# Kernel optimization log

Hardware: AMD Instinct MI355X
Metric: run time of the kernel (lower is better)

The kernel has to match this reference:

```python
import jax, jax.numpy as jnp
import numpy as np


def conv2d(x, w, b, pad=0, groups=1):
    y = jax.lax.conv_general_dilated(
        x, w, (1, 1), [(pad, pad), (pad, pad)],
        dimension_numbers=('NCHW', 'OIHW', 'NCHW'), feature_group_count=groups)
    return y + b[None, :, None, None]


def layernorm(x, w, b, eps=1e-5):
    # per-pixel LayerNorm over channel dim (matches to_3d -> nn.LayerNorm(dim) -> to_4d)
    mu = x.mean(1, keepdims=True)
    var = ((x - mu) ** 2).mean(1, keepdims=True)
    return (x - mu) * jax.lax.rsqrt(var + eps) * w[None, :, None, None] + b[None, :, None, None]


def setup_inputs():
    key = jax.random.key(0)
    ks = jax.random.split(key, 16)
    B, C, H, W = 1, 64, 64, 64
    heads, dh = 8, 8
    inner = heads * dh          # 64
    hid_lc = 32                 # max(16, inner // 2)
    hid_f = 4 * C               # 256, ffn_expansion_factor = 4
    def s(k, shape, fan):
        return (jax.random.normal(k, shape, jnp.float32) / np.float32(np.sqrt(fan)))
    return {
        'x': jax.random.normal(ks[0], (B, C, H, W), jnp.float32),
        'luma': jax.random.uniform(ks[1], (B, 1, H, W), jnp.float32),
        'ln1_w': jnp.ones((C,), jnp.float32), 'ln1_b': jnp.zeros((C,), jnp.float32),
        'qkv_w': s(ks[2], (3 * inner, C, 1, 1), C), 'qkv_b': jnp.zeros((3 * inner,), jnp.float32),
        'proj_w': s(ks[3], (C, inner, 1, 1), inner), 'proj_b': jnp.zeros((C,), jnp.float32),
        'lc1_w': s(ks[4], (hid_lc, 1, 3, 3), 9), 'lc1_b': jnp.zeros((hid_lc,), jnp.float32),
        'lc2_w': s(ks[5], (hid_lc, hid_lc, 3, 3), 9 * hid_lc), 'lc2_b': jnp.zeros((hid_lc,), jnp.float32),
        'gam_w': s(ks[6], (inner, hid_lc, 1, 1), hid_lc), 'gam_b': jnp.zeros((inner,), jnp.float32),
        'bet_w': s(ks[7], (inner, hid_lc, 1, 1), hid_lc), 'bet_b': jnp.zeros((inner,), jnp.float32),
        'alpha': jnp.float32(0.1),
        'ln2_w': jnp.ones((C,), jnp.float32), 'ln2_b': jnp.zeros((C,), jnp.float32),
        'ffn1_w': s(ks[8], (hid_f, C, 1, 1), C), 'ffn1_b': jnp.zeros((hid_f,), jnp.float32),
        'dw_w': s(ks[9], (hid_f, 1, 3, 3), 9), 'dw_b': jnp.zeros((hid_f,), jnp.float32),
        'ffn2_w': s(ks[10], (C, hid_f, 1, 1), hid_f), 'ffn2_b': jnp.zeros((C,), jnp.float32),
    }


def reference(x, luma, ln1_w, ln1_b, qkv_w, qkv_b, proj_w, proj_b,
              lc1_w, lc1_b, lc2_w, lc2_b, gam_w, gam_b, bet_w, bet_b, alpha,
              ln2_w, ln2_b, ffn1_w, ffn1_b, dw_w, dw_b, ffn2_w, ffn2_b):
    B, C, H, W = x.shape
    heads = 8
    N = H * W
    # --- attention branch ---
    xn = layernorm(x, ln1_w, ln1_b)
    qkv = conv2d(xn, qkv_w, qkv_b)             # [B, 3*inner, H, W]
    inner = qkv.shape[1] // 3
    dh = inner // heads

    def to_bhnd(t):  # b (h d) x y -> b h (x y) d
        return t.reshape(B, heads, dh, N).transpose(0, 1, 3, 2)

    q, k, v = [to_bhnd(t) for t in jnp.split(qkv, 3, axis=1)]
    # luma conditioning
    h1 = jax.nn.relu(conv2d(luma, lc1_w, lc1_b, pad=1))
    h1 = jax.nn.relu(conv2d(h1, lc2_w, lc2_b, pad=1))
    g = to_bhnd(conv2d(h1, gam_w, gam_b))
    bt = to_bhnd(conv2d(h1, bet_w, bet_b))
    q = g * q + bt
    k = g * k + bt
    v = g * v + bt
    # additive luma bias on q (avg_pool2d 3x3, count_include_pad=True -> fixed /9)
    invL = 1.0 - luma
    invL = jax.lax.reduce_window(invL, 0.0, jax.lax.add, (1, 1, 3, 3), (1, 1, 1, 1),
                                 [(0, 0), (0, 0), (1, 1), (1, 1)]) / 9.0
    invL = invL.reshape(B, N)
    invL = invL - invL.mean(-1, keepdims=True)
    q = q + alpha * invL[:, None, :, None]
    scale = dh ** -0.5
    attn = jax.nn.softmax(jnp.einsum('bhid,bhjd->bhij', q, k) * scale, axis=-1)
    out = jnp.einsum('bhij,bhjd->bhid', attn, v)
    out = out.transpose(0, 1, 3, 2).reshape(B, inner, H, W)
    x = x + conv2d(out, proj_w, proj_b)
    # --- ConvFFN branch ---
    y = layernorm(x, ln2_w, ln2_b)
    y = conv2d(y, ffn1_w, ffn1_b)
    y = conv2d(y, dw_w, dw_b, pad=1, groups=y.shape[1])
    y = jax.nn.gelu(y, approximate=False)
    y = conv2d(y, ffn2_w, ffn2_b)
    return x + y
```

## Files before the change

kernel.cpp:

```cpp
#include <hip/hip_runtime.h>
#include <math.h>

#define NPIX 4096
#define IMG 64

typedef __attribute__((ext_vector_type(8))) short bf16x8;
typedef __attribute__((ext_vector_type(4))) float floatx4;
typedef __attribute__((ext_vector_type(4))) unsigned int uintx4;

__device__ __forceinline__ unsigned int split_pack(float x) {
  unsigned int u = __float_as_uint(x);
  unsigned int hif = u & 0xffff0000u;
  float lof = x - __uint_as_float(hif);
  return (u >> 16) | (__float_as_uint(lof) & 0xffff0000u);
}

__device__ __forceinline__ unsigned int hi_pair(float a, float b) {
  return (__float_as_uint(a) >> 16) | (__float_as_uint(b) & 0xffff0000u);
}

__global__ __launch_bounds__(256) void lc1_kernel(
    const float* __restrict__ luma, const float* __restrict__ w1,
    const float* __restrict__ b1, float* __restrict__ h1,
    float* __restrict__ pooled, float* __restrict__ bsums,
    unsigned short* __restrict__ cbuf) {
  __shared__ float red[256];
  int tile = blockIdx.x, ocg = blockIdx.y;
  int tid = threadIdx.x;
  if (tile == 0 && ocg == 0 && tid < 16) cbuf[tid] = (tid < 8) ? 0x3F80 : 0;
  int p = tile * 256 + tid;
  int py = p >> 6, px = p & 63;
  float v[9];
#pragma unroll
  for (int dy = 0; dy < 3; dy++)
#pragma unroll
    for (int dx = 0; dx < 3; dx++) {
      int y = py + dy - 1, x = px + dx - 1;
      v[dy * 3 + dx] =
          (y >= 0 && y < IMG && x >= 0 && x < IMG) ? luma[y * IMG + x] : 0.f;
    }
#pragma unroll
  for (int o = 0; o < 4; o++) {
    int oc = ocg * 4 + o;
    float s = b1[oc];
#pragma unroll
    for (int t = 0; t < 9; t++) s = fmaf(w1[oc * 9 + t], v[t], s);
    h1[oc * NPIX + p] = fmaxf(s, 0.f);
  }
  if (ocg == 0) {
    float sv = 0.f;
#pragma unroll
    for (int t = 0; t < 9; t++) sv += v[t];
    float cy = 3.f - (py == 0 ? 1.f : 0.f) - (py == 63 ? 1.f : 0.f);
    float cx = 3.f - (px == 0 ? 1.f : 0.f) - (px == 63 ? 1.f : 0.f);
    float pv = (cy * cx - sv) * (1.f / 9.f);
    pooled[p] = pv;
    red[tid] = pv;
    __syncthreads();
    for (int st = 128; st > 0; st >>= 1) {
      if (tid < st) red[tid] += red[tid + st];
      __syncthreads();
    }
    if (tid == 0) bsums[tile] = red[0];
  }
}

__global__ __launch_bounds__(256) void lc2_kernel(
    const float* __restrict__ h1, const float* __restrict__ w2,
    const float* __restrict__ b2, const float* __restrict__ x,
    float* __restrict__ h2, float* __restrict__ mu1, float* __restrict__ rs1) {
  __shared__ float tin[32][324];
  __shared__ float swt[4][32][9];
  int tile = blockIdx.x, ocg = blockIdx.y;
  int ty0 = (tile >> 2) * 16, tx0 = (tile & 3) * 16;
  int tid = threadIdx.x;
  for (int idx = tid; idx < 32 * 324; idx += 256) {
    int ic = idx / 324, pos = idx - ic * 324;
    int py = pos / 18, px = pos - py * 18;
    int gy = ty0 + py - 1, gx = tx0 + px - 1;
    tin[ic][pos] = (gy >= 0 && gy < IMG && gx >= 0 && gx < IMG)
                       ? h1[ic * NPIX + gy * IMG + gx]
                       : 0.f;
  }
  for (int idx = tid; idx < 4 * 32 * 9; idx += 256) {
    int o = idx / 288, r = idx - o * 288;
    swt[o][r / 9][r % 9] = w2[(ocg * 4 + o) * 288 + r];
  }
  __syncthreads();
  int ly = tid >> 4, lx = tid & 15;
  int p = (ty0 + ly) * IMG + tx0 + lx;
  float acc[4];
#pragma unroll
  for (int o = 0; o < 4; o++) acc[o] = b2[ocg * 4 + o];
  for (int ic = 0; ic < 32; ic++) {
    float v[9];
#pragma unroll
    for (int dy = 0; dy < 3; dy++)
#pragma unroll
      for (int dx = 0; dx < 3; dx++)
        v[dy * 3 + dx] = tin[ic][(ly + dy) * 18 + lx + dx];
#pragma unroll
    for (int o = 0; o < 4; o++)
#pragma unroll
      for (int t = 0; t < 9; t++) acc[o] = fmaf(swt[o][ic][t], v[t], acc[o]);
  }
#pragma unroll
  for (int o = 0; o < 4; o++)
    h2[(ocg * 4 + o) * NPIX + p] = fmaxf(acc[o], 0.f);
  if (ocg == 0) {
    float s = 0.f, q = 0.f;
#pragma unroll 8
    for (int cc = 0; cc < 64; cc++) {
      float xv = x[cc * NPIX + p];
      s += xv;
      q = fmaf(xv, xv, q);
    }
    float mu = s * (1.f / 64.f);
    mu1[p] = mu;
    rs1[p] = rsqrtf(q * (1.f / 64.f) - mu * mu + 1e-5f);
  }
}

__global__ __launch_bounds__(256) void ln_qkv_kernel(
    const float* __restrict__ X, const float* __restrict__ mu1,
    const float* __restrict__ rs1, const float* __restrict__ lnw,
    const float* __restrict__ lnb, const float* __restrict__ W,
    const float* __restrict__ bias, const float* __restrict__ gamW,
    const float* __restrict__ gamB, const float* __restrict__ betW,
    const float* __restrict__ betB, const float* __restrict__ h2,
    const float* __restrict__ pooled, const float* __restrict__ bsums,
    const float* __restrict__ alpha, unsigned short* __restrict__ qhl,
    unsigned short* __restrict__ khl, unsigned short* __restrict__ vthx,
    unsigned short* __restrict__ vtlx) {
  const float QSCALE = 0.35355339059327376f * 1.4426950408889634f;
  __shared__ float xs[64][64];
  __shared__ float wsh[64][64];
  __shared__ float h2s[32][64];
  __shared__ float wgs[32][64];
  __shared__ float wbs[32][64];
  __shared__ float mu[64];
  __shared__ float rs[64];
  int n0 = blockIdx.x * 64, part = blockIdx.y, m0 = part * 64;
  int tid = threadIdx.x;
  int c = tid >> 2, pg = (tid & 3) * 16;
  if (tid < 64) {
    mu[tid] = mu1[n0 + tid];
    rs[tid] = rs1[n0 + tid];
  }
  {
    const float4* src = (const float4*)&X[c * NPIX + n0 + pg];
    float4* dst = (float4*)&xs[c][pg];
    dst[0] = src[0]; dst[1] = src[1]; dst[2] = src[2]; dst[3] = src[3];
  }
  {
    int m = tid >> 2, kg = (tid & 3) * 16;
    const float4* wr = (const float4*)&W[(m0 + m) * 64 + kg];
    float4 w0 = wr[0], w1 = wr[1], w2 = wr[2], w3 = wr[3];
    float wv[16] = {w0.x, w0.y, w0.z, w0.w, w1.x, w1.y, w1.z, w1.w,
                    w2.x, w2.y, w2.z, w2.w, w3.x, w3.y, w3.z, w3.w};
#pragma unroll
    for (int j = 0; j < 16; j++) wsh[kg + j][m] = wv[j];
  }
  {
    int i0 = tid * 2;
    int k = i0 >> 4, nf = (i0 & 15) * 4;
    *(float4*)&h2s[k][nf] = *(const float4*)&h2[k * NPIX + n0 + nf];
    int i1 = i0 + 1;
    int k1 = i1 >> 4, nf1 = (i1 & 15) * 4;
    *(float4*)&h2s[k1][nf1] = *(const float4*)&h2[k1 * NPIX + n0 + nf1];
  }
  {
    int m = tid >> 2, kg = (tid & 3) * 8;
    const float4* g0 = (const float4*)&gamW[m * 32 + kg];
    float4 a = g0[0], b4 = g0[1];
    float gv[8] = {a.x, a.y, a.z, a.w, b4.x, b4.y, b4.z, b4.w};
#pragma unroll
    for (int j = 0; j < 8; j++) wgs[kg + j][m] = gv[j];
    const float4* bb0 = (const float4*)&betW[m * 32 + kg];
    float4 c4 = bb0[0], d4 = bb0[1];
    float bv[8] = {c4.x, c4.y, c4.z, c4.w, d4.x, d4.y, d4.z, d4.w};
#pragma unroll
    for (int j = 0; j < 8; j++) wbs[kg + j][m] = bv[j];
  }
  __syncthreads();
  {
    float wc = lnw[c], bc = lnb[c];
#pragma unroll
    for (int j = 0; j < 16; j++) {
      int p = pg + j;
      xs[c][p] = (xs[c][p] - mu[p]) * rs[p] * wc + bc;
    }
  }
  __syncthreads();
  int tx = tid & 15, ty = tid >> 4;
  float ga[4][4] = {}, ba[4][4] = {};
#pragma unroll 8
  for (int kk = 0; kk < 32; kk++) {
    float4 wg4 = *(const float4*)&wgs[kk][ty * 4];
    float4 wb4 = *(const float4*)&wbs[kk][ty * 4];
    float4 h24 = *(const float4*)&h2s[kk][tx * 4];
    float gv[4] = {wg4.x, wg4.y, wg4.z, wg4.w};
    float bv[4] = {wb4.x, wb4.y, wb4.z, wb4.w};
    float hv[4] = {h24.x, h24.y, h24.z, h24.w};
#pragma unroll
    for (int im = 0; im < 4; im++)
#pragma unroll
      for (int in = 0; in < 4; in++) {
        ga[im][in] = fmaf(gv[im], hv[in], ga[im][in]);
        ba[im][in] = fmaf(bv[im], hv[in], ba[im][in]);
      }
  }
#pragma unroll
  for (int im = 0; im < 4; im++) {
    int cc = ty * 4 + im;
    float gb = gamB[cc], bb2 = betB[cc];
#pragma unroll
    for (int in = 0; in < 4; in++) {
      ga[im][in] += gb;
      ba[im][in] += bb2;
    }
  }
  float acc[4][4] = {};
#pragma unroll 8
  for (int kk = 0; kk < 64; kk++) {
    float4 a = *(const float4*)&wsh[kk][ty * 4];
    float4 b4 = *(const float4*)&xs[kk][tx * 4];
    float av[4] = {a.x, a.y, a.z, a.w};
    float bv[4] = {b4.x, b4.y, b4.z, b4.w};
#pragma unroll
    for (int im = 0; im < 4; im++)
#pragma unroll
      for (int in = 0; in < 4; in++)
        acc[im][in] = fmaf(av[im], bv[in], acc[im][in]);
  }
  float val[4][4];
#pragma unroll
  for (int im = 0; im < 4; im++) {
    int cc = ty * 4 + im;
    float bv = bias[m0 + cc];
#pragma unroll
    for (int in = 0; in < 4; in++)
      val[im][in] = fmaf(ga[im][in], acc[im][in] + bv, ba[im][in]);
  }
  if (part == 0) {
    float msum = 0.f;
#pragma unroll
    for (int t = 0; t < 16; t++) msum += bsums[t];
    float mean = msum * (1.f / 4096.f);
    float a0 = alpha[0];
    const float4 pv = *(const float4*)&pooled[n0 + tx * 4];
    float iv[4] = {a0 * (pv.x - mean), a0 * (pv.y - mean),
                   a0 * (pv.z - mean), a0 * (pv.w - mean)};
#pragma unroll
    for (int im = 0; im < 4; im++)
#pragma unroll
      for (int in = 0; in < 4; in++)
        val[im][in] = (val[im][in] + iv[in]) * QSCALE;
  }
  if (part < 2) {
    unsigned short* dst = (part == 0) ? qhl : khl;
    int h = ty >> 1, d0 = (ty & 1) * 4;
#pragma unroll
    for (int in = 0; in < 4; in++) {
      int n = n0 + tx * 4 + in;
      unsigned int pk[4];
#pragma unroll
      for (int im = 0; im < 4; im++) pk[im] = split_pack(val[im][in]);
      short4 hi, lo;
      hi.x = (short)(pk[0] & 0xffffu); hi.y = (short)(pk[1] & 0xffffu);
      hi.z = (short)(pk[2] & 0xffffu); hi.w = (short)(pk[3] & 0xffffu);
      lo.x = (short)(pk[0] >> 16); lo.y = (short)(pk[1] >> 16);
      lo.z = (short)(pk[2] >> 16); lo.w = (short)(pk[3] >> 16);
      unsigned short* base = dst + ((size_t)(h * NPIX + n) << 4) + d0;
      *(short4*)base = hi;
      *(short4*)(base + 8) = lo;
    }
  } else {
    int nq = n0 + tx * 4;
    int off0 = (nq >> 5) * 32 + ((nq >> 4) & 1) * 4 + ((nq >> 2) & 3) * 8;
#pragma unroll
    for (int im = 0; im < 4; im++) {
      int cc = ty * 4 + im;
      unsigned int pk[4];
#pragma unroll
      for (int in = 0; in < 4; in++) pk[in] = split_pack(val[im][in]);
      short4 hi, lo;
      hi.x = (short)(pk[0] & 0xffffu); hi.y = (short)(pk[1] & 0xffffu);
      hi.z = (short)(pk[2] & 0xffffu); hi.w = (short)(pk[3] & 0xffffu);
      lo.x = (short)(pk[0] >> 16); lo.y = (short)(pk[1] >> 16);
      lo.z = (short)(pk[2] >> 16); lo.w = (short)(pk[3] >> 16);
      *(short4*)(vthx + (size_t)cc * NPIX + off0) = hi;
      *(short4*)(vtlx + (size_t)cc * NPIX + off0) = lo;
    }
  }
}

__global__ __launch_bounds__(256, 4) void attn_kernel(
    const unsigned short* __restrict__ qhl,
    const unsigned short* __restrict__ khl,
    const unsigned short* __restrict__ vthx,
    const unsigned short* __restrict__ vtlx,
    const unsigned short* __restrict__ cbuf, float* __restrict__ pacc,
    float* __restrict__ pl) {
  int tid = threadIdx.x;
  int wave = tid >> 6, lane = tid & 63;
  int g = lane >> 4, c = lane & 15;
  int h = blockIdx.y, jp = blockIdx.z;
  int i0 = blockIdx.x * 128 + wave * 32;
  int jbase = jp * 1024;
  const bf16x8 qB0 = *(const bf16x8*)(qhl + ((size_t)(h * NPIX + i0 + c) << 4) +
                                      ((g & 1) << 3));
  const bf16x8 qB1 = *(const bf16x8*)(
      qhl + ((size_t)(h * NPIX + i0 + 16 + c) << 4) + ((g & 1) << 3));
  const unsigned short* kp =
      khl + ((size_t)(h * NPIX + jbase + c) << 4) + ((g >> 1) << 3);
  const unsigned short* vhp;
  const unsigned short* vlp;
  int vstep;
  if (c < 8) {
    vhp = vthx + (size_t)(h * 8 + c) * NPIX + jbase + (g << 3);
    vlp = vtlx + (size_t)(h * 8 + c) * NPIX + jbase + (g << 3);
    vstep = 32;
  } else {
    vhp = (c == 8) ? cbuf : (cbuf + 8);
    vlp = cbuf + 8;
    vstep = 0;
  }
  floatx4 zero4 = {0.f, 0.f, 0.f, 0.f};
  floatx4 aH0 = zero4, aM0 = zero4, aH1 = zero4, aM1 = zero4;
#pragma unroll 2
  for (int jt = 0; jt < 32; ++jt) {
    bf16x8 ka0 = *(const bf16x8*)kp;
    bf16x8 ka1 = *(const bf16x8*)(kp + 256);
    bf16x8 avh = *(const bf16x8*)vhp;
    bf16x8 avl = *(const bf16x8*)vlp;
    kp += 512;
    vhp += vstep;
    vlp += vstep;
    floatx4 s00 =
        __builtin_amdgcn_mfma_f32_16x16x32_bf16(ka0, qB0, zero4, 0, 0, 0);
    floatx4 s01 =
        __builtin_amdgcn_mfma_f32_16x16x32_bf16(ka1, qB0, zero4, 0, 0, 0);
    floatx4 s10 =
        __builtin_amdgcn_mfma_f32_16x16x32_bf16(ka0, qB1, zero4, 0, 0, 0);
    floatx4 s11 =
        __builtin_amdgcn_mfma_f32_16x16x32_bf16(ka1, qB1, zero4, 0, 0, 0);
    {
      float p0 = __builtin_amdgcn_exp2f(fminf(s00[0], 80.f));
      float p1 = __builtin_amdgcn_exp2f(fminf(s00[1], 80.f));
      float p2 = __builtin_amdgcn_exp2f(fminf(s00[2], 80.f));
      float p3 = __builtin_amdgcn_exp2f(fminf(s00[3], 80.f));
      float p4 = __builtin_amdgcn_exp2f(fminf(s01[0], 80.f));
      float p5 = __builtin_amdgcn_exp2f(fminf(s01[1], 80.f));
      float p6 = __builtin_amdgcn_exp2f(fminf(s01[2], 80.f));
      float p7 = __builtin_amdgcn_exp2f(fminf(s01[3], 80.f));
      uintx4 bh;
      bh.x = hi_pair(p0, p1);
      bh.y = hi_pair(p2, p3);
      bh.z = hi_pair(p4, p5);
      bh.w = hi_pair(p6, p7);
      bf16x8 pbh = __builtin_bit_cast(bf16x8, bh);
      aH0 = __builtin_amdgcn_mfma_f32_16x16x32_bf16(avh, pbh, aH0, 0, 0, 0);
      aM0 = __builtin_amdgcn_mfma_f32_16x16x32_bf16(avl, pbh, aM0, 0, 0, 0);
    }
    {
      float p0 = __builtin_amdgcn_exp2f(fminf(s10[0], 80.f));
      float p1 = __builtin_amdgcn_exp2f(fminf(s10[1], 80.f));
      float p2 = __builtin_amdgcn_exp2f(fminf(s10[2], 80.f));
      float p3 = __builtin_amdgcn_exp2f(fminf(s10[3], 80.f));
      float p4 = __builtin_amdgcn_exp2f(fminf(s11[0], 80.f));
      float p5 = __builtin_amdgcn_exp2f(fminf(s11[1], 80.f));
      float p6 = __builtin_amdgcn_exp2f(fminf(s11[2], 80.f));
      float p7 = __builtin_amdgcn_exp2f(fminf(s11[3], 80.f));
      uintx4 bh;
      bh.x = hi_pair(p0, p1);
      bh.y = hi_pair(p2, p3);
      bh.z = hi_pair(p4, p5);
      bh.w = hi_pair(p6, p7);
      bf16x8 pbh = __builtin_bit_cast(bf16x8, bh);
      aH1 = __builtin_amdgcn_mfma_f32_16x16x32_bf16(avh, pbh, aH1, 0, 0, 0);
      aM1 = __builtin_amdgcn_mfma_f32_16x16x32_bf16(avl, pbh, aM1, 0, 0, 0);
    }
  }
  floatx4 o0 = aH0 + aM0;
  floatx4 o1 = aH1 + aM1;
  if (g < 2) {
    size_t b0 = (size_t)((jp * 8 + h) * NPIX + i0 + c);
    *(float4*)&pacc[b0 * 8 + g * 4] = make_float4(o0[0], o0[1], o0[2], o0[3]);
    size_t b1 = b0 + 16;
    *(float4*)&pacc[b1 * 8 + g * 4] = make_float4(o1[0], o1[1], o1[2], o1[3]);
  } else if (g == 2) {
    pl[(size_t)((jp * 8 + h) * NPIX + i0 + c)] = o0[0];
    pl[(size_t)((jp * 8 + h) * NPIX + i0 + 16 + c)] = o1[0];
  }
}

__global__ __launch_bounds__(256) void proj_ffn1_kernel(
    const float* __restrict__ pacc, const float* __restrict__ pl,
    const float* __restrict__ Wp, const float* __restrict__ bp,
    const float* __restrict__ x, const float* __restrict__ ln2w,
    const float* __restrict__ ln2b, const float* __restrict__ W1,
    const float* __restrict__ b1f, float* __restrict__ x1,
    float* __restrict__ f1) {
  __shared__ float at[64][33];
  __shared__ float wsh[64][64];
  __shared__ float xsl[64][33];
  __shared__ float ps[8][33];
  __shared__ float pq[8][33];
  __shared__ float mus[32];
  __shared__ float rss[32];
  int n0 = blockIdx.x * 32;
  int ch = blockIdx.y;
  int tid = threadIdx.x;
  {
    int mm = tid >> 2, kg = (tid & 3) * 16;
    const float4* wr = (const float4*)&Wp[mm * 64 + kg];
    float4 w0 = wr[0], w1 = wr[1], w2 = wr[2], w3 = wr[3];
    float wv[16] = {w0.x, w0.y, w0.z, w0.w, w1.x, w1.y, w1.z, w1.w,
                    w2.x, w2.y, w2.z, w2.w, w3.x, w3.y, w3.z, w3.w};
#pragma unroll
    for (int j = 0; j < 16; j++) wsh[kg + j][mm] = wv[j];
  }
  {
    int hh = tid >> 5, nn = tid & 31;
    int i = n0 + nn;
    float L = 0.f, o[8] = {};
#pragma unroll
    for (int p = 0; p < 4; p++) {
      size_t base = (size_t)((p * 8 + hh) * NPIX + i);
      L += pl[base];
      const float4 a0 = *(const float4*)&pacc[base * 8];
      const float4 a1 = *(const float4*)&pacc[base * 8 + 4];
      o[0] += a0.x; o[1] += a0.y; o[2] += a0.z; o[3] += a0.w;
      o[4] += a1.x; o[5] += a1.y; o[6] += a1.z; o[7] += a1.w;
    }
    float inv = 1.f / L;
#pragma unroll
    for (int d = 0; d < 8; d++) at[hh * 8 + d][nn] = o[d] * inv;
  }
  __syncthreads();
  int ty = tid >> 5, tx = tid & 31;
  float acc[8] = {};
#pragma unroll 8
  for (int k = 0; k < 64; k++) {
    float b = at[k][tx];
    float4 a0 = *(const float4*)&wsh[k][ty * 8];
    float4 a1 = *(const float4*)&wsh[k][ty * 8 + 4];
    acc[0] = fmaf(a0.x, b, acc[0]);
    acc[1] = fmaf(a0.y, b, acc[1]);
    acc[2] = fmaf(a0.z, b, acc[2]);
    acc[3] = fmaf(a0.w, b, acc[3]);
    acc[4] = fmaf(a1.x, b, acc[4]);
    acc[5] = fmaf(a1.y, b, acc[5]);
    acc[6] = fmaf(a1.z, b, acc[6]);
    acc[7] = fmaf(a1.w, b, acc[7]);
  }
  float v[8], sn = 0.f, qn = 0.f;
#pragma unroll
  for (int im = 0; im < 8; im++) {
    int row = ty * 8 + im;
    float vv = acc[im] + bp[row] + x[row * NPIX + n0 + tx];
    v[im] = vv;
    sn += vv;
    qn = fmaf(vv, vv, qn);
  }
  if (ch == 0) {
#pragma unroll
    for (int im = 0; im < 8; im++)
      x1[(ty * 8 + im) * NPIX + n0 + tx] = v[im];
  }
  ps[ty][tx] = sn;
  pq[ty][tx] = qn;
  __syncthreads();
  if (tid < 32) {
    float s = 0.f, q = 0.f;
#pragma unroll
    for (int t = 0; t < 8; t++) {
      s += ps[t][tid];
      q += pq[t][tid];
    }
    float mu = s * (1.f / 64.f);
    mus[tid] = mu;
    rss[tid] = rsqrtf(q * (1.f / 64.f) - mu * mu + 1e-5f);
  }
  __syncthreads();
  {
    float muv = mus[tx], rsv = rss[tx];
#pragma unroll
    for (int im = 0; im < 8; im++) {
      int row = ty * 8 + im;
      xsl[row][tx] = (v[im] - muv) * rsv * ln2w[row] + ln2b[row];
    }
  }
  {
    int mm = tid >> 2, kg = (tid & 3) * 16;
    const float4* wr = (const float4*)&W1[(ch * 64 + mm) * 64 + kg];
    float4 w0 = wr[0], w1 = wr[1], w2 = wr[2], w3 = wr[3];
    float wv[16] = {w0.x, w0.y, w0.z, w0.w, w1.x, w1.y, w1.z, w1.w,
                    w2.x, w2.y, w2.z, w2.w, w3.x, w3.y, w3.z, w3.w};
#pragma unroll
    for (int j = 0; j < 16; j++) wsh[kg + j][mm] = wv[j];
  }
  __syncthreads();
  float a2[8] = {};
#pragma unroll 8
  for (int k = 0; k < 64; k++) {
    float b = xsl[k][tx];
    float4 a0 = *(const float4*)&wsh[k][ty * 8];
    float4 a1 = *(const float4*)&wsh[k][ty * 8 + 4];
    a2[0] = fmaf(a0.x, b, a2[0]);
    a2[1] = fmaf(a0.y, b, a2[1]);
    a2[2] = fmaf(a0.z, b, a2[2]);
    a2[3] = fmaf(a0.w, b, a2[3]);
    a2[4] = fmaf(a1.x, b, a2[4]);
    a2[5] = fmaf(a1.y, b, a2[5]);
    a2[6] = fmaf(a1.z, b, a2[6]);
    a2[7] = fmaf(a1.w, b, a2[7]);
  }
#pragma unroll
  for (int im = 0; im < 8; im++) {
    int row = ch * 64 + ty * 8 + im;
    f1[row * NPIX + n0 + tx] = a2[im] + b1f[row];
  }
}

__global__ __launch_bounds__(256) void dw_gelu_kernel(
    const float* __restrict__ f1, const float* __restrict__ w,
    const float* __restrict__ b, float* __restrict__ f2) {
  int t = blockIdx.x * 256 + threadIdx.x;
  int c = t >> 10, pq = t & 1023;
  int py = pq >> 4, px0 = (pq & 15) << 2;
  const float* base = f1 + c * NPIX;
  float wv[9];
#pragma unroll
  for (int i = 0; i < 9; i++) wv[i] = w[c * 9 + i];
  float bc = b[c];
  float a[4] = {bc, bc, bc, bc};
#pragma unroll
  for (int dy = 0; dy < 3; dy++) {
    int y = py + dy - 1;
    if (y < 0 || y > 63) continue;
    const float* row = base + y * IMG + px0;
    float4 mid = *(const float4*)row;
    float left = (px0 > 0) ? row[-1] : 0.f;
    float right = (px0 < 60) ? row[4] : 0.f;
    float win[6] = {left, mid.x, mid.y, mid.z, mid.w, right};
#pragma unroll
    for (int o = 0; o < 4; o++)
#pragma unroll
      for (int dx = 0; dx < 3; dx++)
        a[o] = fmaf(wv[dy * 3 + dx], win[o + dx], a[o]);
  }
  float4 o4;
  float* op = &o4.x;
#pragma unroll
  for (int o = 0; o < 4; o++)
    op[o] = 0.5f * a[o] * (1.f + erff(a[o] * 0.70710678118654752f));
  *(float4*)&f2[c * NPIX + py * IMG + px0] = o4;
}

__global__ __launch_bounds__(256) void ffn2_kernel(
    const float* __restrict__ W, const float* __restrict__ X,
    const float* __restrict__ bias, const float* __restrict__ resid,
    float* __restrict__ C) {
  __shared__ float xs[256][32];
  __shared__ float wsh[256][16];
  int n0 = blockIdx.x * 32, m0 = blockIdx.y * 16;
  int tid = threadIdx.x;
#pragma unroll
  for (int e = tid; e < 2048; e += 256) {
    int k = e >> 3, nf = (e & 7) * 4;
    *(float4*)&xs[k][nf] = *(const float4*)&X[k * NPIX + n0 + nf];
  }
#pragma unroll
  for (int e = tid; e < 4096; e += 256) {
    int mm = e >> 8, kk = e & 255;
    wsh[kk][mm] = W[(m0 + mm) * 256 + kk];
  }
  __syncthreads();
  int m = tid >> 4, np = (tid & 15) * 2;
  float acc0 = 0.f, acc1 = 0.f;
#pragma unroll 8
  for (int kk = 0; kk < 256; kk++) {
    float a = wsh[kk][m];
    float2 b2 = *(const float2*)&xs[kk][np];
    acc0 = fmaf(a, b2.x, acc0);
    acc1 = fmaf(a, b2.y, acc1);
  }
  int row = m0 + m;
  float bv = bias[row];
  const float2 r2 = *(const float2*)&resid[row * NPIX + n0 + np];
  float2 o = make_float2(acc0 + bv + r2.x, acc1 + bv + r2.y);
  *(float2*)&C[row * NPIX + n0 + np] = o;
}

extern "C" void kernel_launch(void* const* d_in, const int* in_sizes, int n_in,
                              void* d_out, int out_size, void* d_ws,
                              size_t ws_size, hipStream_t stream) {
  const float* x      = (const float*)d_in[0];
  const float* luma   = (const float*)d_in[1];
  const float* ln1_w  = (const float*)d_in[2];
  const float* ln1_b  = (const float*)d_in[3];
  const float* qkv_w  = (const float*)d_in[4];
  const float* qkv_b  = (const float*)d_in[5];
  const float* proj_w = (const float*)d_in[6];
  const float* proj_b = (const float*)d_in[7];
  const float* lc1_w  = (const float*)d_in[8];
  const float* lc1_b  = (const float*)d_in[9];
  const float* lc2_w  = (const float*)d_in[10];
  const float* lc2_b  = (const float*)d_in[11];
  const float* gam_w  = (const float*)d_in[12];
  const float* gam_b  = (const float*)d_in[13];
  const float* bet_w  = (const float*)d_in[14];
  const float* bet_b  = (const float*)d_in[15];
  const float* alpha  = (const float*)d_in[16];
  const float* ln2_w  = (const float*)d_in[17];
  const float* ln2_b  = (const float*)d_in[18];
  const float* ffn1_w = (const float*)d_in[19];
  const float* ffn1_b = (const float*)d_in[20];
  const float* dw_w   = (const float*)d_in[21];
  const float* dw_b   = (const float*)d_in[22];
  const float* ffn2_w = (const float*)d_in[23];
  const float* ffn2_b = (const float*)d_in[24];
  float* out = (float*)d_out;

  float* w = (float*)d_ws;
  float* pooled = w + 0;
  float* bsums  = w + 4096;
  unsigned short* cbuf = (unsigned short*)(w + 4160);
  float* mu1 = w + 4224;
  float* rs1 = w + 8320;
  unsigned short* qhl  = (unsigned short*)(w + 12416);
  unsigned short* khl  = (unsigned short*)(w + 274560);
  unsigned short* vthx = (unsigned short*)(w + 536704);
  unsigned short* vtlx = (unsigned short*)(w + 667776);
  float* pacc = w + 798848;
  float* pl   = w + 1847424;
  float* x1   = w + 1978496;
  float* f1   = w + 2240640;
  float* f2   = w + 3289216;
  float* h2   = w + 4337792;
  float* h1   = w + 4468864;

  lc1_kernel<<<dim3(16, 8), 256, 0, stream>>>(luma, lc1_w, lc1_b, h1, pooled,
                                              bsums, cbuf);
  lc2_kernel<<<dim3(16, 8), 256, 0, stream>>>(h1, lc2_w, lc2_b, x, h2, mu1,
                                              rs1);
  ln_qkv_kernel<<<dim3(64, 3), 256, 0, stream>>>(
      x, mu1, rs1, ln1_w, ln1_b, qkv_w, qkv_b, gam_w, gam_b, bet_w, bet_b, h2,
      pooled, bsums, alpha, qhl, khl, vthx, vtlx);
  attn_kernel<<<dim3(32, 8, 4), 256, 0, stream>>>(qhl, khl, vthx, vtlx, cbuf,
                                                  pacc, pl);
  proj_ffn1_kernel<<<dim3(128, 4), 256, 0, stream>>>(
      pacc, pl, proj_w, proj_b, x, ln2_w, ln2_b, ffn1_w, ffn1_b, x1, f1);
  dw_gelu_kernel<<<1024, 256, 0, stream>>>(f1, dw_w, dw_b, f2);
  ffn2_kernel<<<dim3(128, 4), 256, 0, stream>>>(ffn2_w, f2, ffn2_b, x1, out);
}
```

Baseline: 202.6 us.

## Retile attention to 64 queries per wave with 8-way key split, halve qkv tile

The attention kernel now keeps four 16-row query fragments per wave instead of two. This doubles reuse of each loaded K/V fragment across the MFMA calls. The key dimension is split into 8 partitions of 512 instead of 4 of 1024, so the grid shape stays the same while partial output buffers double, and proj_ffn1 now reduces 8 partials. The ln_qkv kernel moves to 32-pixel tiles with twice as many blocks to raise occupancy. The trade-off is more register pressure in attention and more partial-sum traffic.

```diff
diff --git a/kernel.cpp b/kernel.cpp
--- a/kernel.cpp
+++ b/kernel.cpp
@@ -133,24 +133,26 @@
     unsigned short* __restrict__ khl, unsigned short* __restrict__ vthx,
     unsigned short* __restrict__ vtlx) {
   const float QSCALE = 0.35355339059327376f * 1.4426950408889634f;
-  __shared__ float xs[64][64];
+  __shared__ float xs[64][32];
   __shared__ float wsh[64][64];
-  __shared__ float h2s[32][64];
+  __shared__ float h2s[32][32];
   __shared__ float wgs[32][64];
   __shared__ float wbs[32][64];
-  __shared__ float mu[64];
-  __shared__ float rs[64];
-  int n0 = blockIdx.x * 64, part = blockIdx.y, m0 = part * 64;
+  __shared__ float mu[32];
+  __shared__ float rs[32];
+  int n0 = blockIdx.x * 32, part = blockIdx.y, m0 = part * 64;
   int tid = threadIdx.x;
-  int c = tid >> 2, pg = (tid & 3) * 16;
-  if (tid < 64) {
+  if (tid < 32) {
     mu[tid] = mu1[n0 + tid];
     rs[tid] = rs1[n0 + tid];
   }
   {
-    const float4* src = (const float4*)&X[c * NPIX + n0 + pg];
-    float4* dst = (float4*)&xs[c][pg];
-    dst[0] = src[0]; dst[1] = src[1]; dst[2] = src[2]; dst[3] = src[3];
+    int e = tid * 2;
+    int c = e >> 3, off = (e & 7) * 4;
+    *(float4*)&xs[c][off] = *(const float4*)&X[c * NPIX + n0 + off];
+    int e1 = e + 1;
+    int c1 = e1 >> 3, off1 = (e1 & 7) * 4;
+    *(float4*)&xs[c1][off1] = *(const float4*)&X[c1 * NPIX + n0 + off1];
   }
   {
     int m = tid >> 2, kg = (tid & 3) * 16;
@@ -162,12 +164,8 @@
     for (int j = 0; j < 16; j++) wsh[kg + j][m] = wv[j];
   }
   {
-    int i0 = tid * 2;
-    int k = i0 >> 4, nf = (i0 & 15) * 4;
+    int k = tid >> 3, nf = (tid & 7) * 4;
     *(float4*)&h2s[k][nf] = *(const float4*)&h2[k * NPIX + n0 + nf];
-    int i1 = i0 + 1;
-    int k1 = i1 >> 4, nf1 = (i1 & 15) * 4;
-    *(float4*)&h2s[k1][nf1] = *(const float4*)&h2[k1 * NPIX + n0 + nf1];
   }
   {
     int m = tid >> 2, kg = (tid & 3) * 8;
@@ -184,28 +182,29 @@
   }
   __syncthreads();
   {
+    int c = tid >> 2, pg = (tid & 3) * 8;
     float wc = lnw[c], bc = lnb[c];
 #pragma unroll
-    for (int j = 0; j < 16; j++) {
+    for (int j = 0; j < 8; j++) {
       int p = pg + j;
       xs[c][p] = (xs[c][p] - mu[p]) * rs[p] * wc + bc;
     }
   }
   __syncthreads();
   int tx = tid & 15, ty = tid >> 4;
-  float ga[4][4] = {}, ba[4][4] = {};
+  float ga[4][2] = {}, ba[4][2] = {};
 #pragma unroll 8
   for (int kk = 0; kk < 32; kk++) {
     float4 wg4 = *(const float4*)&wgs[kk][ty * 4];
     float4 wb4 = *(const float4*)&wbs[kk][ty * 4];
-    float4 h24 = *(const float4*)&h2s[kk][tx * 4];
+    float2 h22 = *(const float2*)&h2s[kk][tx * 2];
     float gv[4] = {wg4.x, wg4.y, wg4.z, wg4.w};
     float bv[4] = {wb4.x, wb4.y, wb4.z, wb4.w};
-    float hv[4] = {h24.x, h24.y, h24.z, h24.w};
+    float hv[2] = {h22.x, h22.y};
 #pragma unroll
     for (int im = 0; im < 4; im++)
 #pragma unroll
-      for (int in = 0; in < 4; in++) {
+      for (int in = 0; in < 2; in++) {
         ga[im][in] = fmaf(gv[im], hv[in], ga[im][in]);
         ba[im][in] = fmaf(bv[im], hv[in], ba[im][in]);
       }
@@ -215,31 +214,31 @@
     int cc = ty * 4 + im;
     float gb = gamB[cc], bb2 = betB[cc];
 #pragma unroll
-    for (int in = 0; in < 4; in++) {
+    for (int in = 0; in < 2; in++) {
       ga[im][in] += gb;
       ba[im][in] += bb2;
     }
   }
-  float acc[4][4] = {};
+  float acc[4][2] = {};
 #pragma unroll 8
   for (int kk = 0; kk < 64; kk++) {
     float4 a = *(const float4*)&wsh[kk][ty * 4];
-    float4 b4 = *(const float4*)&xs[kk][tx * 4];
+    float2 b2 = *(const float2*)&xs[kk][tx * 2];
     float av[4] = {a.x, a.y, a.z, a.w};
-    float bv[4] = {b4.x, b4.y, b4.z, b4.w};
+    float bv[2] = {b2.x, b2.y};
 #pragma unroll
     for (int im = 0; im < 4; im++)
 #pragma unroll
-      for (int in = 0; in < 4; in++)
+      for (int in = 0; in < 2; in++)
         acc[im][in] = fmaf(av[im], bv[in], acc[im][in]);
   }
-  float val[4][4];
+  float val[4][2];
 #pragma unroll
   for (int im = 0; im < 4; im++) {
     int cc = ty * 4 + im;
     float bv = bias[m0 + cc];
 #pragma unroll
-    for (int in = 0; in < 4; in++)
+    for (int in = 0; in < 2; in++)
       val[im][in] = fmaf(ga[im][in], acc[im][in] + bv, ba[im][in]);
   }
   if (part == 0) {
@@ -248,21 +247,20 @@
     for (int t = 0; t < 16; t++) msum += bsums[t];
     float mean = msum * (1.f / 4096.f);
     float a0 = alpha[0];
-    const float4 pv = *(const float4*)&pooled[n0 + tx * 4];
-    float iv[4] = {a0 * (pv.x - mean), a0 * (pv.y - mean),
-                   a0 * (pv.z - mean), a0 * (pv.w - mean)};
+    const float2 pv = *(const float2*)&pooled[n0 + tx * 2];
+    float iv[2] = {a0 * (pv.x - mean), a0 * (pv.y - mean)};
 #pragma unroll
     for (int im = 0; im < 4; im++)
 #pragma unroll
-      for (int in = 0; in < 4; in++)
+      for (int in = 0; in < 2; in++)
         val[im][in] = (val[im][in] + iv[in]) * QSCALE;
   }
   if (part < 2) {
     unsigned short* dst = (part == 0) ? qhl : khl;
     int h = ty >> 1, d0 = (ty & 1) * 4;
 #pragma unroll
-    for (int in = 0; in < 4; in++) {
-      int n = n0 + tx * 4 + in;
+    for (int in = 0; in < 2; in++) {
+      int n = n0 + tx * 2 + in;
       unsigned int pk[4];
 #pragma unroll
       for (int im = 0; im < 4; im++) pk[im] = split_pack(val[im][in]);
@@ -276,21 +274,21 @@
       *(short4*)(base + 8) = lo;
     }
   } else {
-    int nq = n0 + tx * 4;
-    int off0 = (nq >> 5) * 32 + ((nq >> 4) & 1) * 4 + ((nq >> 2) & 3) * 8;
+    int nq = n0 + tx * 2;
+    int off0 = (nq >> 5) * 32 + ((nq >> 4) & 1) * 4 + ((nq >> 2) & 3) * 8 +
+               (nq & 3);
 #pragma unroll
     for (int im = 0; im < 4; im++) {
       int cc = ty * 4 + im;
-      unsigned int pk[4];
-#pragma unroll
-      for (int in = 0; in < 4; in++) pk[in] = split_pack(val[im][in]);
-      short4 hi, lo;
-      hi.x = (short)(pk[0] & 0xffffu); hi.y = (short)(pk[1] & 0xffffu);
-      hi.z = (short)(pk[2] & 0xffffu); hi.w = (short)(pk[3] & 0xffffu);
-      lo.x = (short)(pk[0] >> 16); lo.y = (short)(pk[1] >> 16);
-      lo.z = (short)(pk[2] >> 16); lo.w = (short)(pk[3] >> 16);
-      *(short4*)(vthx + (size_t)cc * NPIX + off0) = hi;
-      *(short4*)(vtlx + (size_t)cc * NPIX + off0) = lo;
+      unsigned int pk0 = split_pack(val[im][0]);
+      unsigned int pk1 = split_pack(val[im][1]);
+      short2 hi, lo;
+      hi.x = (short)(pk0 & 0xffffu);
+      hi.y = (short)(pk1 & 0xffffu);
+      lo.x = (short)(pk0 >> 16);
+      lo.y = (short)(pk1 >> 16);
+      *(short2*)(vthx + (size_t)cc * NPIX + off0) = hi;
+      *(short2*)(vtlx + (size_t)cc * NPIX + off0) = lo;
     }
   }
 }
@@ -306,12 +304,13 @@
   int wave = tid >> 6, lane = tid & 63;
   int g = lane >> 4, c = lane & 15;
   int h = blockIdx.y, jp = blockIdx.z;
-  int i0 = blockIdx.x * 128 + wave * 32;
-  int jbase = jp * 1024;
-  const bf16x8 qB0 = *(const bf16x8*)(qhl + ((size_t)(h * NPIX + i0 + c) << 4) +
-                                      ((g & 1) << 3));
-  const bf16x8 qB1 = *(const bf16x8*)(
-      qhl + ((size_t)(h * NPIX + i0 + 16 + c) << 4) + ((g & 1) << 3));
+  int i0 = blockIdx.x * 256 + wave * 64;
+  int jbase = jp * 512;
+  bf16x8 qB[4];
+#pragma unroll
+  for (int t = 0; t < 4; t++)
+    qB[t] = *(const bf16x8*)(qhl + ((size_t)(h * NPIX + i0 + t * 16 + c) << 4) +
+                             ((g & 1) << 3));
   const unsigned short* kp =
       khl + ((size_t)(h * NPIX + jbase + c) << 4) + ((g >> 1) << 3);
   const unsigned short* vhp;
@@ -327,9 +326,14 @@
     vstep = 0;
   }
   floatx4 zero4 = {0.f, 0.f, 0.f, 0.f};
-  floatx4 aH0 = zero4, aM0 = zero4, aH1 = zero4, aM1 = zero4;
+  floatx4 aH[4], aM[4];
+#pragma unroll
+  for (int t = 0; t < 4; t++) {
+    aH[t] = zero4;
+    aM[t] = zero4;
+  }
 #pragma unroll 2
-  for (int jt = 0; jt < 32; ++jt) {
+  for (int jt = 0; jt < 16; ++jt) {
     bf16x8 ka0 = *(const bf16x8*)kp;
     bf16x8 ka1 = *(const bf16x8*)(kp + 256);
     bf16x8 avh = *(const bf16x8*)vhp;
@@ -337,61 +341,39 @@
     kp += 512;
     vhp += vstep;
     vlp += vstep;
-    floatx4 s00 =
-        __builtin_amdgcn_mfma_f32_16x16x32_bf16(ka0, qB0, zero4, 0, 0, 0);
-    floatx4 s01 =
-        __builtin_amdgcn_mfma_f32_16x16x32_bf16(ka1, qB0, zero4, 0, 0, 0);
-    floatx4 s10 =
-        __builtin_amdgcn_mfma_f32_16x16x32_bf16(ka0, qB1, zero4, 0, 0, 0);
-    floatx4 s11 =
-        __builtin_amdgcn_mfma_f32_16x16x32_bf16(ka1, qB1, zero4, 0, 0, 0);
-    {
-      float p0 = __builtin_amdgcn_exp2f(fminf(s00[0], 80.f));
-      float p1 = __builtin_amdgcn_exp2f(fminf(s00[1], 80.f));
-      float p2 = __builtin_amdgcn_exp2f(fminf(s00[2], 80.f));
-      float p3 = __builtin_amdgcn_exp2f(fminf(s00[3], 80.f));
-      float p4 = __builtin_amdgcn_exp2f(fminf(s01[0], 80.f));
-      float p5 = __builtin_amdgcn_exp2f(fminf(s01[1], 80.f));
-      float p6 = __builtin_amdgcn_exp2f(fminf(s01[2], 80.f));
-      float p7 = __builtin_amdgcn_exp2f(fminf(s01[3], 80.f));
+#pragma unroll
+    for (int t = 0; t < 4; t++) {
+      floatx4 s0 =
+          __builtin_amdgcn_mfma_f32_16x16x32_bf16(ka0, qB[t], zero4, 0, 0, 0);
+      floatx4 s1 =
+          __builtin_amdgcn_mfma_f32_16x16x32_bf16(ka1, qB[t], zero4, 0, 0, 0);
+      float p0 = __builtin_amdgcn_exp2f(fminf(s0[0], 80.f));
+      float p1 = __builtin_amdgcn_exp2f(fminf(s0[1], 80.f));
+      float p2 = __builtin_amdgcn_exp2f(fminf(s0[2], 80.f));
+      float p3 = __builtin_amdgcn_exp2f(fminf(s0[3], 80.f));
+      float p4 = __builtin_amdgcn_exp2f(fminf(s1[0], 80.f));
+      float p5 = __builtin_amdgcn_exp2f(fminf(s1[1], 80.f));
+      float p6 = __builtin_amdgcn_exp2f(fminf(s1[2], 80.f));
+      float p7 = __builtin_amdgcn_exp2f(fminf(s1[3], 80.f));
       uintx4 bh;
       bh.x = hi_pair(p0, p1);
       bh.y = hi_pair(p2, p3);
       bh.z = hi_pair(p4, p5);
       bh.w = hi_pair(p6, p7);
       bf16x8 pbh = __builtin_bit_cast(bf16x8, bh);
-      aH0 = __builtin_amdgcn_mfma_f32_16x16x32_bf16(avh, pbh, aH0, 0, 0, 0);
-      aM0 = __builtin_amdgcn_mfma_f32_16x16x32_bf16(avl, pbh, aM0, 0, 0, 0);
-    }
-    {
-      float p0 = __builtin_amdgcn_exp2f(fminf(s10[0], 80.f));
-      float p1 = __builtin_amdgcn_exp2f(fminf(s10[1], 80.f));
-      float p2 = __builtin_amdgcn_exp2f(fminf(s10[2], 80.f));
-      float p3 = __builtin_amdgcn_exp2f(fminf(s10[3], 80.f));
-      float p4 = __builtin_amdgcn_exp2f(fminf(s11[0], 80.f));
-      float p5 = __builtin_amdgcn_exp2f(fminf(s11[1], 80.f));
-      float p6 = __builtin_amdgcn_exp2f(fminf(s11[2], 80.f));
-      float p7 = __builtin_amdgcn_exp2f(fminf(s11[3], 80.f));
-      uintx4 bh;
-      bh.x = hi_pair(p0, p1);
-      bh.y = hi_pair(p2, p3);
-      bh.z = hi_pair(p4, p5);
-      bh.w = hi_pair(p6, p7);
-      bf16x8 pbh = __builtin_bit_cast(bf16x8, bh);
-      aH1 = __builtin_amdgcn_mfma_f32_16x16x32_bf16(avh, pbh, aH1, 0, 0, 0);
-      aM1 = __builtin_amdgcn_mfma_f32_16x16x32_bf16(avl, pbh, aM1, 0, 0, 0);
-    }
-  }
-  floatx4 o0 = aH0 + aM0;
-  floatx4 o1 = aH1 + aM1;
-  if (g < 2) {
-    size_t b0 = (size_t)((jp * 8 + h) * NPIX + i0 + c);
-    *(float4*)&pacc[b0 * 8 + g * 4] = make_float4(o0[0], o0[1], o0[2], o0[3]);
-    size_t b1 = b0 + 16;
-    *(float4*)&pacc[b1 * 8 + g * 4] = make_float4(o1[0], o1[1], o1[2], o1[3]);
-  } else if (g == 2) {
-    pl[(size_t)((jp * 8 + h) * NPIX + i0 + c)] = o0[0];
-    pl[(size_t)((jp * 8 + h) * NPIX + i0 + 16 + c)] = o1[0];
+      aH[t] = __builtin_amdgcn_mfma_f32_16x16x32_bf16(avh, pbh, aH[t], 0, 0, 0);
+      aM[t] = __builtin_amdgcn_mfma_f32_16x16x32_bf16(avl, pbh, aM[t], 0, 0, 0);
+    }
+  }
+#pragma unroll
+  for (int t = 0; t < 4; t++) {
+    floatx4 o = aH[t] + aM[t];
+    if (g < 2) {
+      size_t b0 = (size_t)((jp * 8 + h) * NPIX + i0 + t * 16 + c);
+      *(float4*)&pacc[b0 * 8 + g * 4] = make_float4(o[0], o[1], o[2], o[3]);
+    } else if (g == 2) {
+      pl[(size_t)((jp * 8 + h) * NPIX + i0 + t * 16 + c)] = o[0];
+    }
   }
 }
 
@@ -426,7 +408,7 @@
     int i = n0 + nn;
     float L = 0.f, o[8] = {};
 #pragma unroll
-    for (int p = 0; p < 4; p++) {
+    for (int p = 0; p < 8; p++) {
       size_t base = (size_t)((p * 8 + hh) * NPIX + i);
       L += pl[base];
       const float4 a0 = *(const float4*)&pacc[base * 8];
@@ -635,21 +617,21 @@
   unsigned short* vthx = (unsigned short*)(w + 536704);
   unsigned short* vtlx = (unsigned short*)(w + 667776);
   float* pacc = w + 798848;
-  float* pl   = w + 1847424;
-  float* x1   = w + 1978496;
-  float* f1   = w + 2240640;
-  float* f2   = w + 3289216;
-  float* h2   = w + 4337792;
-  float* h1   = w + 4468864;
+  float* pl   = w + 2896000;
+  float* x1   = w + 3158144;
+  float* f1   = w + 3420288;
+  float* f2   = w + 4468864;
+  float* h2   = w + 5517440;
+  float* h1   = w + 5648512;
 
   lc1_kernel<<<dim3(16, 8), 256, 0, stream>>>(luma, lc1_w, lc1_b, h1, pooled,
                                               bsums, cbuf);
   lc2_kernel<<<dim3(16, 8), 256, 0, stream>>>(h1, lc2_w, lc2_b, x, h2, mu1,
                                               rs1);
-  ln_qkv_kernel<<<dim3(64, 3), 256, 0, stream>>>(
+  ln_qkv_kernel<<<dim3(128, 3), 256, 0, stream>>>(
       x, mu1, rs1, ln1_w, ln1_b, qkv_w, qkv_b, gam_w, gam_b, bet_w, bet_b, h2,
       pooled, bsums, alpha, qhl, khl, vthx, vtlx);
-  attn_kernel<<<dim3(32, 8, 4), 256, 0, stream>>>(qhl, khl, vthx, vtlx, cbuf,
+  attn_kernel<<<dim3(16, 8, 8), 256, 0, stream>>>(qhl, khl, vthx, vtlx, cbuf,
                                                   pacc, pl);
   proj_ffn1_kernel<<<dim3(128, 4), 256, 0, stream>>>(
       pacc, pl, proj_w, proj_b, x, ln2_w, ln2_b, ffn1_w, ffn1_b, x1, f1);
```

Measured after the change: 202.5 us. Within noise of the previous version (-0.1%).
